# Kernel optimization log

Hardware: AMD Instinct MI355X
Metric: run time of the kernel (lower is better)

## Reference

```python
import jax, jax.numpy as jnp
import numpy as np

N = 65536        # number of encoding vectors (flattened tokens)
K = 1024         # num_embeddings (codebook size)
D = 128          # embedding_dim
BETA = 0.25


def setup_inputs() -> dict:
    key = jax.random.key(0)
    k_enc, k_cb = jax.random.split(key)
    encoding = jax.random.normal(k_enc, (N, D), dtype=jnp.float32)
    # nn.Embedding weight initialized uniform(-1/K, 1/K)
    codebook = jax.random.uniform(k_cb, (K, D), dtype=jnp.float32,
                                  minval=-1.0 / K, maxval=1.0 / K)
    return {"encoding": encoding, "codebook": codebook}


def reference(encoding, codebook):
    # Nearest codebook entry per row. argmin of L2 distance == argmin of
    # squared distance; expand ||e - w||^2 = ||e||^2 - 2 e.w + ||w||^2.
    # ||e||^2 is constant per row, so it does not affect the argmin.
    scores = (-2.0 * jnp.einsum('nd,kd->nk', encoding, codebook)
              + jnp.sum(codebook * codebook, axis=-1)[None, :])  # [N, K]
    quantized_index = jnp.argmin(scores, axis=-1)                # [N] int
    quantized_embedding = codebook[quantized_index]              # [N, D] gather == onehot @ W

    sg = jax.lax.stop_gradient
    commitment_loss = jnp.mean((sg(quantized_embedding) - encoding) ** 2)
    embedding_loss = jnp.mean((quantized_embedding - sg(encoding)) ** 2)
    vq_loss = commitment_loss * BETA + embedding_loss

    # straight-through estimator
    quantized_st = encoding + sg(quantized_embedding - encoding)

    quantized_index = quantized_index[:, None]  # match torch unsqueeze(1) -> [N, 1]
    return (quantized_index, quantized_st, vq_loss, embedding_loss, commitment_loss)
```

## Files before the change

kernel.cpp:

```cpp
#include <hip/hip_runtime.h>


#define NROWS 65536
#define KCB   1024
#define DIM   128
#define DV    32
#define MSE_DENOM 8388608.0f
#define MARGIN 2.0e-5f
#define FLAGCAP 16384
#define CSCALE   1024.0f
#define CDESCALE 0.0009765625f

#define WS_CNORM_F 256
#define WS_LIST_B  8192
#define WS_PH_B    73728
#define WS_PL_B    335872
#define WS_NEEDED  598016

typedef __attribute__((ext_vector_type(16))) float float16v;
typedef _Float16 half8 __attribute__((ext_vector_type(8)));
union U4H8 { uint4 u; half8 h; };
union F4A  { float4 v; float f[4]; };
union HU   { _Float16 f; unsigned short u; };

__device__ __forceinline__ unsigned umn(unsigned a, unsigned b) { return a < b ? a : b; }
__device__ __forceinline__ unsigned umx(unsigned a, unsigned b) { return a > b ? a : b; }
__device__ __forceinline__ float unmap_score(unsigned up) {
  return (up & 0x80000000u) ? __uint_as_float(up ^ 0x80000000u) : __uint_as_float(~up);
}
__device__ __forceinline__ void split2h(float y, unsigned& hb, unsigned& lb) {
  HU h, l;
  h.f = (_Float16)y;
  l.f = (_Float16)(y - (float)h.f);
  hb = h.u; lb = l.u;
}
__device__ __forceinline__ void gload16(const void* g, void* s) {
  __builtin_amdgcn_global_load_lds((const __attribute__((address_space(1))) unsigned int*)g,
                                   (__attribute__((address_space(3))) unsigned int*)s,
                                   16, 0, 0);
}

__global__ __launch_bounds__(256) void vq_prep0(const float* __restrict__ C,
                                                float* __restrict__ wsf) {
  int k = blockIdx.x * 256 + threadIdx.x;
  if (k == 0) { wsf[0] = 0.0f; ((unsigned*)wsf)[1] = 0u; }
  const float4* c4 = (const float4*)C + (size_t)k * DV;
  float s = 0.f;
#pragma unroll 8
  for (int i = 0; i < DV; ++i) {
    float4 v = c4[i];
    s = fmaf(v.x, v.x, s); s = fmaf(v.y, v.y, s);
    s = fmaf(v.z, v.z, s); s = fmaf(v.w, v.w, s);
  }
  wsf[WS_CNORM_F + k] = s;
}

__global__ __launch_bounds__(256) void vq_pack(const float* __restrict__ C,
                                               uint4* __restrict__ PH,
                                               uint4* __restrict__ PL) {
  int g = blockIdx.x * 256 + threadIdx.x;
  int mt = g >> 9, s = (g >> 6) & 7, l = g & 63;
  int cw = mt * 32 + (l & 31);
  int k0 = s * 16 + (l >> 5) * 8;
  const float* src = C + (size_t)cw * DIM + k0;
  float4 x0 = *(const float4*)src;
  float4 x1 = *(const float4*)(src + 4);
  unsigned h[8], lo[8];
  split2h(CSCALE * x0.x, h[0], lo[0]); split2h(CSCALE * x0.y, h[1], lo[1]);
  split2h(CSCALE * x0.z, h[2], lo[2]); split2h(CSCALE * x0.w, h[3], lo[3]);
  split2h(CSCALE * x1.x, h[4], lo[4]); split2h(CSCALE * x1.y, h[5], lo[5]);
  split2h(CSCALE * x1.z, h[6], lo[6]); split2h(CSCALE * x1.w, h[7], lo[7]);
  PH[g] = make_uint4(h[0] | (h[1] << 16), h[2] | (h[3] << 16),
                     h[4] | (h[5] << 16), h[6] | (h[7] << 16));
  PL[g] = make_uint4(lo[0] | (lo[1] << 16), lo[2] | (lo[3] << 16),
                     lo[4] | (lo[5] << 16), lo[6] | (lo[7] << 16));
}

__global__ __launch_bounds__(256, 2) void vq_main3(const float* __restrict__ E,
                                                   const float* __restrict__ C,
                                                   float* __restrict__ wsf,
                                                   float* __restrict__ out) {
  __shared__ uint4 SH[2][512];
  __shared__ uint4 SL[2][512];
  __shared__ __align__(16) float CN[1024];
  __shared__ int BIs[128];

  const int tid  = threadIdx.x;
  const int w    = tid >> 6;
  const int l    = tid & 63;
  const int half = l >> 5;
  const int rr   = l & 31;
  const int row0 = blockIdx.x * 128;

  const uint4* PHg = (const uint4*)((const char*)wsf + WS_PH_B);
  const uint4* PLg = (const uint4*)((const char*)wsf + WS_PL_B);

  {
    const uint4* sh = PHg + tid;
    const uint4* sl = PLg + tid;
    gload16(sh,       &SH[0][0] + tid);
    gload16(sh + 256, &SH[0][0] + tid + 256);
    gload16(sl,       &SL[0][0] + tid);
    gload16(sl + 256, &SL[0][0] + tid + 256);
    gload16(((const uint4*)(wsf + WS_CNORM_F)) + tid, ((uint4*)CN) + tid);
  }

  half8 beh[8], bel[8];
  float s2 = 0.f;
  const float* erow = E + (size_t)(row0 + w * 32 + rr) * DIM + half * 8;
#pragma unroll
  for (int s = 0; s < 8; ++s) {
    float4 x0 = *(const float4*)(erow + s * 16);
    float4 x1 = *(const float4*)(erow + s * 16 + 4);
    float v[8] = {x0.x, x0.y, x0.z, x0.w, x1.x, x1.y, x1.z, x1.w};
#pragma unroll
    for (int j = 0; j < 8; ++j) {
      float y = v[j];
      s2 = fmaf(y, y, s2);
      float t = -2.f * y;
      _Float16 hh = (_Float16)t;
      beh[s][j] = hh;
      bel[s][j] = (_Float16)(t - (float)hh);
    }
  }

  asm volatile("s_waitcnt vmcnt(0)" ::: "memory");
  __syncthreads();

  unsigned best = 0xFFFFFFFFu, second = 0xFFFFFFFFu;

  for (int t = 0; t < 32; ++t) {
    const int buf = t & 1;
    if (t < 31) {
      const uint4* sh = PHg + (t + 1) * 512 + tid;
      const uint4* sl = PLg + (t + 1) * 512 + tid;
      uint4* dh = &SH[buf ^ 1][0];
      uint4* dl = &SL[buf ^ 1][0];
      gload16(sh,       dh + tid);
      gload16(sh + 256, dh + tid + 256);
      gload16(sl,       dl + tid);
      gload16(sl + 256, dl + tid + 256);
    }

    float16v acc0 = {0,0,0,0,0,0,0,0,0,0,0,0,0,0,0,0};
    float16v acc1 = {0,0,0,0,0,0,0,0,0,0,0,0,0,0,0,0};
#pragma unroll
    for (int s = 0; s < 8; s += 2) {
      U4H8 h0, l0, h1, l1;
      h0.u = SH[buf][s * 64 + l];       l0.u = SL[buf][s * 64 + l];
      h1.u = SH[buf][(s + 1) * 64 + l]; l1.u = SL[buf][(s + 1) * 64 + l];
      acc0 = __builtin_amdgcn_mfma_f32_32x32x16_f16(h0.h, beh[s],     acc0, 0, 0, 0);
      acc1 = __builtin_amdgcn_mfma_f32_32x32x16_f16(h1.h, beh[s + 1], acc1, 0, 0, 0);
      acc0 = __builtin_amdgcn_mfma_f32_32x32x16_f16(l0.h, beh[s],     acc0, 0, 0, 0);
      acc1 = __builtin_amdgcn_mfma_f32_32x32x16_f16(l1.h, beh[s + 1], acc1, 0, 0, 0);
      acc0 = __builtin_amdgcn_mfma_f32_32x32x16_f16(h0.h, bel[s],     acc0, 0, 0, 0);
      acc1 = __builtin_amdgcn_mfma_f32_32x32x16_f16(h1.h, bel[s + 1], acc1, 0, 0, 0);
    }

    const unsigned cwb = (unsigned)(t * 32 + half * 4);
    float cnv[16];
#pragma unroll
    for (int q = 0; q < 4; ++q) {
      F4A a; a.v = *(const float4*)&CN[t * 32 + q * 8 + half * 4];
      cnv[q * 4 + 0] = a.f[0]; cnv[q * 4 + 1] = a.f[1];
      cnv[q * 4 + 2] = a.f[2]; cnv[q * 4 + 3] = a.f[3];
    }
#pragma unroll
    for (int reg = 0; reg < 16; ++reg) {
      float sc = fmaf(acc0[reg] + acc1[reg], CDESCALE, cnv[reg]);
      unsigned u = __float_as_uint(sc);
      u ^= ((unsigned)(((int)u) >> 31)) | 0x80000000u;
      u = (u & 0xFFFFFC00u) | (cwb + (unsigned)(((reg >> 2) * 8) + (reg & 3)));
      unsigned nb = umn(best, u);
      second = umn(second, umx(best, u));
      best = nb;
    }

    asm volatile("s_waitcnt vmcnt(0)" ::: "memory");
    __syncthreads();
  }

  unsigned ob = (unsigned)__shfl_xor((int)best, 32, 64);
  unsigned os = (unsigned)__shfl_xor((int)second, 32, 64);
  unsigned ns = umn(umn(second, os), umx(best, ob));
  unsigned nb = umn(best, ob);
  float en = s2 + __shfl_xor(s2, 32, 64);

  if (half == 0) {
    const int r = w * 32 + rr;
    int   bi = (int)(nb & 1023u);
    float bv = unmap_score(nb & 0xFFFFFC00u);
    float sv = unmap_score(ns & 0xFFFFFC00u);
    out[row0 + r] = (float)bi;
    BIs[r] = bi;
    if (sv - bv < MARGIN) {
      unsigned idx = atomicAdd((unsigned*)wsf + 1, 1u);
      if (idx < FLAGCAP) ((int*)((char*)wsf + WS_LIST_B))[idx] = row0 + r;
    }
    float term = en + bv;
#pragma unroll
    for (int off = 16; off > 0; off >>= 1) term += __shfl_down(term, off);
    if (rr == 0) atomicAdd(wsf, term);
  }
  __syncthreads();

  const float4* C4   = (const float4*)C;
  float4*       out4 = (float4*)out;
#pragma unroll
  for (int it = 0; it < 16; ++it) {
    int flat = it * 256 + tid;
    int r = flat >> 5, d4 = flat & 31;
    out4[(NROWS / 4) + (size_t)(row0 + r) * DV + d4] = C4[(size_t)BIs[r] * DV + d4];
  }
}

__global__ __launch_bounds__(256) void vq_fix(const float* __restrict__ E,
                                              const float* __restrict__ C,
                                              float* __restrict__ wsf,
                                              float* __restrict__ out) {
  __shared__ float4 eL0[32], eL1[32];
  __shared__ float  sv0[256], sv1[256];
  __shared__ int    si0[256], si1[256];
  __shared__ int    RESi[2];
  const int tid = threadIdx.x;
  const int* list = (const int*)((const char*)wsf + WS_LIST_B);
  int nf = (int)((const unsigned*)wsf)[1];
  if (nf > FLAGCAP) nf = FLAGCAP;
  const float4* E4 = (const float4*)E;
  const float4* C4 = (const float4*)C;
  const float*  cn = wsf + WS_CNORM_F;
  float4* out4 = (float4*)out;

  for (int pair = blockIdx.x; pair * 2 < nf; pair += gridDim.x) {
    const int r0 = list[pair * 2];
    const int r1 = (pair * 2 + 1 < nf) ? list[pair * 2 + 1] : r0;
    if (tid < 32) eL0[tid] = E4[(size_t)r0 * DV + tid];
    else if (tid < 64) eL1[tid - 32] = E4[(size_t)r1 * DV + (tid - 32)];
    __syncthreads();
    float bv0 = 3.0e38f, bv1 = 3.0e38f; int bi0 = 0, bi1 = 0;
#pragma unroll
    for (int j = 0; j < 4; ++j) {
      int k = j * 256 + tid;
      float d0 = 0.f, d1 = 0.f;
#pragma unroll 8
      for (int d4 = 0; d4 < 32; ++d4) {
        float4 c = C4[(size_t)k * DV + d4];
        float4 e0 = eL0[d4], e1 = eL1[d4];
        d0 = fmaf(c.x, e0.x, d0); d0 = fmaf(c.y, e0.y, d0);
        d0 = fmaf(c.z, e0.z, d0); d0 = fmaf(c.w, e0.w, d0);
        d1 = fmaf(c.x, e1.x, d1); d1 = fmaf(c.y, e1.y, d1);
        d1 = fmaf(c.z, e1.z, d1); d1 = fmaf(c.w, e1.w, d1);
      }
      float s0 = fmaf(-2.f, d0, cn[k]);
      float s1 = fmaf(-2.f, d1, cn[k]);
      if (s0 < bv0 || (s0 == bv0 && k < bi0)) { bv0 = s0; bi0 = k; }
      if (s1 < bv1 || (s1 == bv1 && k < bi1)) { bv1 = s1; bi1 = k; }
    }
    sv0[tid] = bv0; si0[tid] = bi0; sv1[tid] = bv1; si1[tid] = bi1;
    __syncthreads();
    if (tid < 64) {
      float v0 = sv0[tid]; int i0 = si0[tid];
      float v1 = sv1[tid]; int i1 = si1[tid];
#pragma unroll
      for (int q = 1; q < 4; ++q) {
        float w0 = sv0[tid + q * 64]; int j0 = si0[tid + q * 64];
        float w1 = sv1[tid + q * 64]; int j1 = si1[tid + q * 64];
        if (w0 < v0 || (w0 == v0 && j0 < i0)) { v0 = w0; i0 = j0; }
        if (w1 < v1 || (w1 == v1 && j1 < i1)) { v1 = w1; i1 = j1; }
      }
#pragma unroll
      for (int off = 32; off > 0; off >>= 1) {
        float w0 = __shfl_down(v0, off); int j0 = __shfl_down(i0, off);
        float w1 = __shfl_down(v1, off); int j1 = __shfl_down(i1, off);
        if (w0 < v0 || (w0 == v0 && j0 < i0)) { v0 = w0; i0 = j0; }
        if (w1 < v1 || (w1 == v1 && j1 < i1)) { v1 = w1; i1 = j1; }
      }
      if (tid == 0) {
        RESi[0] = i0; RESi[1] = i1;
        out[r0] = (float)i0; out[r1] = (float)i1;
      }
    }
    __syncthreads();
    if (tid < 32) out4[(NROWS / 4) + (size_t)r0 * DV + tid] = C4[(size_t)RESi[0] * DV + tid];
    else if (tid < 64) out4[(NROWS / 4) + (size_t)r1 * DV + (tid - 32)] = C4[(size_t)RESi[1] * DV + (tid - 32)];
    __syncthreads();
  }
}

__global__ void vq_final(const float* __restrict__ wsf, float* __restrict__ out) {
  if (threadIdx.x == 0 && blockIdx.x == 0) {
    float mse = wsf[0] / MSE_DENOM;
    out[NROWS + NROWS * DIM + 0] = 1.25f * mse;
    out[NROWS + NROWS * DIM + 1] = mse;
    out[NROWS + NROWS * DIM + 2] = mse;
  }
}

__global__ __launch_bounds__(256) void vq_prep_fb(const float* __restrict__ C,
                                                  float* __restrict__ ws) {
  int k = blockIdx.x * 256 + threadIdx.x;
  if (k == 0) ws[0] = 0.0f;
  const float4* c4 = (const float4*)C + (size_t)k * DV;
  float s = 0.f;
#pragma unroll 8
  for (int i = 0; i < DV; ++i) {
    float4 v = c4[i];
    s = fmaf(v.x, v.x, s); s = fmaf(v.y, v.y, s);
    s = fmaf(v.z, v.z, s); s = fmaf(v.w, v.w, s);
  }
  ws[64 + k] = s;
}

__global__ __launch_bounds__(256) void vq_main_fb(const float* __restrict__ E,
                                                  const float* __restrict__ C,
                                                  const float* __restrict__ cnorm,
                                                  float* __restrict__ out,
                                                  float* __restrict__ lossacc) {
  __shared__ float smem[16384];
  float4* EsV = (float4*)smem;
  float4* CsV = (float4*)(smem + 8192);
  const int tid  = threadIdx.x;
  const int row0 = blockIdx.x * 64;
#pragma unroll
  for (int i = 0; i < 8; ++i) {
    int flat = i * 256 + tid;
    int r = flat >> 5, d4 = flat & 31;
    EsV[r * 32 + (d4 ^ (r & 31))] = ((const float4*)E)[(size_t)(row0 + r) * DV + d4];
  }
  const int tx = tid & 15, ty = tid >> 4;
  int rbase[4], rmask[4];
#pragma unroll
  for (int i = 0; i < 4; ++i) { int r = i * 16 + ty; rbase[i] = r * 32; rmask[i] = r & 31; }
  float bestv[4]; int besti[4];
#pragma unroll
  for (int i = 0; i < 4; ++i) { bestv[i] = 3.0e38f; besti[i] = 0; }
  for (int ch = 0; ch < 16; ++ch) {
    const int k0 = ch * 64;
    __syncthreads();
#pragma unroll
    for (int i = 0; i < 8; ++i) {
      int flat = i * 256 + tid;
      int k = flat >> 5, d4 = flat & 31;
      CsV[k * 32 + (d4 ^ (k & 31))] = ((const float4*)C)[(size_t)(k0 + k) * DV + d4];
    }
    __syncthreads();
    float acc[4][4] = {};
#pragma unroll 8
    for (int d4 = 0; d4 < DV; ++d4) {
      float4 a[4], b[4];
#pragma unroll
      for (int i = 0; i < 4; ++i) a[i] = EsV[rbase[i] + (d4 ^ rmask[i])];
#pragma unroll
      for (int j = 0; j < 4; ++j) { int k = j * 16 + tx; b[j] = CsV[k * 32 + (d4 ^ (k & 31))]; }
#pragma unroll
      for (int i = 0; i < 4; ++i)
#pragma unroll
        for (int j = 0; j < 4; ++j) {
          acc[i][j] = fmaf(a[i].x, b[j].x, acc[i][j]);
          acc[i][j] = fmaf(a[i].y, b[j].y, acc[i][j]);
          acc[i][j] = fmaf(a[i].z, b[j].z, acc[i][j]);
          acc[i][j] = fmaf(a[i].w, b[j].w, acc[i][j]);
        }
    }
#pragma unroll
    for (int j = 0; j < 4; ++j) {
      int kg = k0 + j * 16 + tx;
      float cnv = cnorm[kg];
#pragma unroll
      for (int i = 0; i < 4; ++i) {
        float s = fmaf(-2.0f, acc[i][j], cnv);
        if (s < bestv[i] || (s == bestv[i] && kg < besti[i])) { bestv[i] = s; besti[i] = kg; }
      }
    }
  }
  float* Rv = smem + 8192;
  int*   Ri = (int*)(smem + 9216);
  int*   BIf = (int*)(smem + 10240);
  __syncthreads();
#pragma unroll
  for (int i = 0; i < 4; ++i) {
    int r = i * 16 + ty;
    Rv[r * 16 + tx] = bestv[i];
    Ri[r * 16 + tx] = besti[i];
  }
  __syncthreads();
  if (tid < 64) {
    const int r = tid;
    float bv = Rv[r * 16]; int bi = Ri[r * 16];
#pragma unroll
    for (int t = 1; t < 16; ++t) {
      float v = Rv[r * 16 + t]; int ii = Ri[r * 16 + t];
      if (v < bv || (v == bv && ii < bi)) { bv = v; bi = ii; }
    }
    float en = 0.f;
#pragma unroll 8
    for (int d4 = 0; d4 < DV; ++d4) {
      float4 v = EsV[r * 32 + (d4 ^ (r & 31))];
      en = fmaf(v.x, v.x, en); en = fmaf(v.y, v.y, en);
      en = fmaf(v.z, v.z, en); en = fmaf(v.w, v.w, en);
    }
    out[row0 + r] = (float)bi;
    BIf[r] = bi;
    float blocksum = en + bv;
#pragma unroll
    for (int off = 32; off > 0; off >>= 1) blocksum += __shfl_down(blocksum, off);
    if (tid == 0) atomicAdd(lossacc, blocksum);
  }
  __syncthreads();
  const float4* C4   = (const float4*)C;
  float4*       out4 = (float4*)out;
  for (int flat = tid; flat < 64 * DV; flat += 256) {
    int r = flat >> 5, d4 = flat & 31;
    out4[(NROWS / 4) + (size_t)(row0 + r) * DV + d4] = C4[(size_t)BIf[r] * DV + d4];
  }
}

__global__ void vq_final_fb(const float* __restrict__ ws, float* __restrict__ out) {
  if (threadIdx.x == 0 && blockIdx.x == 0) {
    float mse = ws[0] / MSE_DENOM;
    out[NROWS + NROWS * DIM + 0] = 1.25f * mse;
    out[NROWS + NROWS * DIM + 1] = mse;
    out[NROWS + NROWS * DIM + 2] = mse;
  }
}

extern "C" void kernel_launch(void* const* d_in, const int* in_sizes, int n_in,
                              void* d_out, int out_size, void* d_ws, size_t ws_size,
                              hipStream_t stream) {
  const float* E = (const float*)d_in[0];
  const float* C = (const float*)d_in[1];
  float* out = (float*)d_out;
  float* wsf = (float*)d_ws;

  if (ws_size >= (size_t)WS_NEEDED) {
    uint4* PH = (uint4*)((char*)d_ws + WS_PH_B);
    uint4* PL = (uint4*)((char*)d_ws + WS_PL_B);
    vq_prep0<<<4, 256, 0, stream>>>(C, wsf);
    vq_pack<<<64, 256, 0, stream>>>(C, PH, PL);
    vq_main3<<<NROWS / 128, 256, 0, stream>>>(E, C, wsf, out);
    vq_fix<<<256, 256, 0, stream>>>(E, C, wsf, out);
    vq_final<<<1, 64, 0, stream>>>(wsf, out);
  } else {
    vq_prep_fb<<<4, 256, 0, stream>>>(C, wsf);
    vq_main_fb<<<NROWS / 64, 256, 0, stream>>>(E, C, wsf + 64, out, wsf);
    vq_final_fb<<<1, 64, 0, stream>>>(wsf, out);
  }
}
```

Before: 186.8 us.

## Split codebook search across two blocks per row tile and merge results

Measured after the change: 188.0 us. Within noise of the previous version (+0.6%).

```diff
diff --git a/kernel.cpp b/kernel.cpp
--- a/kernel.cpp
+++ b/kernel.cpp
@@ -76,33 +76,35 @@
                      lo[4] | (lo[5] << 16), lo[6] | (lo[7] << 16));
 }
 
-__global__ __launch_bounds__(256, 2) void vq_main3(const float* __restrict__ E,
-                                                   const float* __restrict__ C,
+__global__ __launch_bounds__(256, 4) void vq_main4(const float* __restrict__ E,
                                                    float* __restrict__ wsf,
                                                    float* __restrict__ out) {
   __shared__ uint4 SH[2][512];
   __shared__ uint4 SL[2][512];
-  __shared__ __align__(16) float CN[1024];
-  __shared__ int BIs[128];
-
-  const int tid  = threadIdx.x;
-  const int w    = tid >> 6;
-  const int l    = tid & 63;
-  const int half = l >> 5;
-  const int rr   = l & 31;
-  const int row0 = blockIdx.x * 128;
+  __shared__ __align__(16) float CN[512];
+
+  const int tid    = threadIdx.x;
+  const int w      = tid >> 6;
+  const int l      = tid & 63;
+  const int half   = l >> 5;
+  const int rr     = l & 31;
+  const int rowblk = blockIdx.x >> 1;
+  const int cbhalf = blockIdx.x & 1;
+  const int row0   = rowblk * 128;
+  const int tgbase = cbhalf * 16;
 
   const uint4* PHg = (const uint4*)((const char*)wsf + WS_PH_B);
   const uint4* PLg = (const uint4*)((const char*)wsf + WS_PL_B);
 
   {
-    const uint4* sh = PHg + tid;
-    const uint4* sl = PLg + tid;
+    const uint4* sh = PHg + (size_t)tgbase * 512 + tid;
+    const uint4* sl = PLg + (size_t)tgbase * 512 + tid;
     gload16(sh,       &SH[0][0] + tid);
     gload16(sh + 256, &SH[0][0] + tid + 256);
     gload16(sl,       &SL[0][0] + tid);
     gload16(sl + 256, &SL[0][0] + tid + 256);
-    gload16(((const uint4*)(wsf + WS_CNORM_F)) + tid, ((uint4*)CN) + tid);
+    if (tid < 128)
+      gload16(((const uint4*)(wsf + WS_CNORM_F + (cbhalf << 9))) + tid, ((uint4*)CN) + tid);
   }
 
   half8 beh[8], bel[8];
@@ -129,11 +131,12 @@
 
   unsigned best = 0xFFFFFFFFu, second = 0xFFFFFFFFu;
 
-  for (int t = 0; t < 32; ++t) {
+  for (int t = 0; t < 16; ++t) {
     const int buf = t & 1;
-    if (t < 31) {
-      const uint4* sh = PHg + (t + 1) * 512 + tid;
-      const uint4* sl = PLg + (t + 1) * 512 + tid;
+    const int tg  = tgbase + t;
+    if (t < 15) {
+      const uint4* sh = PHg + (size_t)(tg + 1) * 512 + tid;
+      const uint4* sl = PLg + (size_t)(tg + 1) * 512 + tid;
       uint4* dh = &SH[buf ^ 1][0];
       uint4* dl = &SL[buf ^ 1][0];
       gload16(sh,       dh + tid);
@@ -157,23 +160,20 @@
       acc1 = __builtin_amdgcn_mfma_f32_32x32x16_f16(h1.h, bel[s + 1], acc1, 0, 0, 0);
     }
 
-    const unsigned cwb = (unsigned)(t * 32 + half * 4);
-    float cnv[16];
+    const unsigned cwb = (unsigned)(tg * 32 + half * 4);
 #pragma unroll
     for (int q = 0; q < 4; ++q) {
       F4A a; a.v = *(const float4*)&CN[t * 32 + q * 8 + half * 4];
-      cnv[q * 4 + 0] = a.f[0]; cnv[q * 4 + 1] = a.f[1];
-      cnv[q * 4 + 2] = a.f[2]; cnv[q * 4 + 3] = a.f[3];
-    }
-#pragma unroll
-    for (int reg = 0; reg < 16; ++reg) {
-      float sc = fmaf(acc0[reg] + acc1[reg], CDESCALE, cnv[reg]);
-      unsigned u = __float_as_uint(sc);
-      u ^= ((unsigned)(((int)u) >> 31)) | 0x80000000u;
-      u = (u & 0xFFFFFC00u) | (cwb + (unsigned)(((reg >> 2) * 8) + (reg & 3)));
-      unsigned nb = umn(best, u);
-      second = umn(second, umx(best, u));
-      best = nb;
+#pragma unroll
+      for (int i = 0; i < 4; ++i) {
+        float sc = fmaf(acc0[q * 4 + i] + acc1[q * 4 + i], CDESCALE, a.f[i]);
+        unsigned u = __float_as_uint(sc);
+        u ^= ((unsigned)(((int)u) >> 31)) | 0x80000000u;
+        u = (u & 0xFFFFFC00u) | (cwb + (unsigned)(q * 8 + i));
+        unsigned nb = umn(best, u);
+        second = umn(second, umx(best, u));
+        best = nb;
+      }
     }
 
     asm volatile("s_waitcnt vmcnt(0)" ::: "memory");
@@ -187,30 +187,52 @@
   float en = s2 + __shfl_xor(s2, 32, 64);
 
   if (half == 0) {
-    const int r = w * 32 + rr;
-    int   bi = (int)(nb & 1023u);
-    float bv = unmap_score(nb & 0xFFFFFC00u);
-    float sv = unmap_score(ns & 0xFFFFFC00u);
-    out[row0 + r] = (float)bi;
-    BIs[r] = bi;
-    if (sv - bv < MARGIN) {
-      unsigned idx = atomicAdd((unsigned*)wsf + 1, 1u);
-      if (idx < FLAGCAP) ((int*)((char*)wsf + WS_LIST_B))[idx] = row0 + r;
-    }
-    float term = en + bv;
-#pragma unroll
-    for (int off = 16; off > 0; off >>= 1) term += __shfl_down(term, off);
-    if (rr == 0) atomicAdd(wsf, term);
-  }
+    const int R = row0 + w * 32 + rr;
+    float* tmp = out + NROWS + (size_t)R * DIM;
+    ((unsigned*)tmp)[cbhalf * 2 + 0] = nb;
+    ((unsigned*)tmp)[cbhalf * 2 + 1] = ns;
+    if (cbhalf == 0) tmp[4] = en;
+  }
+}
+
+__global__ __launch_bounds__(256) void vq_merge(const float* __restrict__ C,
+                                                float* __restrict__ wsf,
+                                                float* __restrict__ out) {
+  __shared__ int BI[256];
+  const int tid  = threadIdx.x;
+  const int row0 = blockIdx.x * 256;
+  const int R    = row0 + tid;
+
+  const float* tmp = out + NROWS + (size_t)R * DIM;
+  unsigned bA = ((const unsigned*)tmp)[0], sA = ((const unsigned*)tmp)[1];
+  unsigned bB = ((const unsigned*)tmp)[2], sB = ((const unsigned*)tmp)[3];
+  float en = tmp[4];
+
+  unsigned b = umn(bA, bB);
+  unsigned s = umn(umn(sA, sB), umx(bA, bB));
+  int   bi = (int)(b & 1023u);
+  float bv = unmap_score(b & 0xFFFFFC00u);
+  float sv = unmap_score(s & 0xFFFFFC00u);
+
+  out[R] = (float)bi;
+  BI[tid] = bi;
+  if (sv - bv < MARGIN) {
+    unsigned idx = atomicAdd((unsigned*)wsf + 1, 1u);
+    if (idx < FLAGCAP) ((int*)((char*)wsf + WS_LIST_B))[idx] = R;
+  }
+  float term = en + bv;
+#pragma unroll
+  for (int off = 32; off > 0; off >>= 1) term += __shfl_down(term, off);
+  if ((tid & 63) == 0) atomicAdd(wsf, term);
   __syncthreads();
 
   const float4* C4   = (const float4*)C;
   float4*       out4 = (float4*)out;
 #pragma unroll
-  for (int it = 0; it < 16; ++it) {
+  for (int it = 0; it < 32; ++it) {
     int flat = it * 256 + tid;
     int r = flat >> 5, d4 = flat & 31;
-    out4[(NROWS / 4) + (size_t)(row0 + r) * DV + d4] = C4[(size_t)BIs[r] * DV + d4];
+    out4[(NROWS / 4) + (size_t)(row0 + r) * DV + d4] = C4[(size_t)BI[r] * DV + d4];
   }
 }
 
@@ -437,8 +459,9 @@
     uint4* PL = (uint4*)((char*)d_ws + WS_PL_B);
     vq_prep0<<<4, 256, 0, stream>>>(C, wsf);
     vq_pack<<<64, 256, 0, stream>>>(C, PH, PL);
-    vq_main3<<<NROWS / 128, 256, 0, stream>>>(E, C, wsf, out);
-    vq_fix<<<256, 256, 0, stream>>>(E, C, wsf, out);
+    vq_main4<<<NROWS / 128 * 2, 256, 0, stream>>>(E, wsf, out);
+    vq_merge<<<NROWS / 256, 256, 0, stream>>>(C, wsf, out);
+    vq_fix<<<512, 256, 0, stream>>>(E, C, wsf, out);
     vq_final<<<1, 64, 0, stream>>>(wsf, out);
   } else {
     vq_prep_fb<<<4, 256, 0, stream>>>(C, wsf);
```

## Drop codebook low-half split, shrink blocks, and software-pipeline the argmin fold

Applied to the files above, without the earlier changes.

After: 167.0 us. -10.6%, faster.

```diff
diff --git a/kernel.cpp b/kernel.cpp
--- a/kernel.cpp
+++ b/kernel.cpp
@@ -14,8 +14,7 @@
 #define WS_CNORM_F 256
 #define WS_LIST_B  8192
 #define WS_PH_B    73728
-#define WS_PL_B    335872
-#define WS_NEEDED  598016
+#define WS_NEEDED  335872
 
 typedef __attribute__((ext_vector_type(16))) float float16v;
 typedef _Float16 half8 __attribute__((ext_vector_type(8)));
@@ -27,12 +26,6 @@
 __device__ __forceinline__ unsigned umx(unsigned a, unsigned b) { return a > b ? a : b; }
 __device__ __forceinline__ float unmap_score(unsigned up) {
   return (up & 0x80000000u) ? __uint_as_float(up ^ 0x80000000u) : __uint_as_float(~up);
-}
-__device__ __forceinline__ void split2h(float y, unsigned& hb, unsigned& lb) {
-  HU h, l;
-  h.f = (_Float16)y;
-  l.f = (_Float16)(y - (float)h.f);
-  hb = h.u; lb = l.u;
 }
 __device__ __forceinline__ void gload16(const void* g, void* s) {
   __builtin_amdgcn_global_load_lds((const __attribute__((address_space(1))) unsigned int*)g,
@@ -56,8 +49,7 @@
 }
 
 __global__ __launch_bounds__(256) void vq_pack(const float* __restrict__ C,
-                                               uint4* __restrict__ PH,
-                                               uint4* __restrict__ PL) {
+                                               uint4* __restrict__ PH) {
   int g = blockIdx.x * 256 + threadIdx.x;
   int mt = g >> 9, s = (g >> 6) & 7, l = g & 63;
   int cw = mt * 32 + (l & 31);
@@ -65,44 +57,42 @@
   const float* src = C + (size_t)cw * DIM + k0;
   float4 x0 = *(const float4*)src;
   float4 x1 = *(const float4*)(src + 4);
-  unsigned h[8], lo[8];
-  split2h(CSCALE * x0.x, h[0], lo[0]); split2h(CSCALE * x0.y, h[1], lo[1]);
-  split2h(CSCALE * x0.z, h[2], lo[2]); split2h(CSCALE * x0.w, h[3], lo[3]);
-  split2h(CSCALE * x1.x, h[4], lo[4]); split2h(CSCALE * x1.y, h[5], lo[5]);
-  split2h(CSCALE * x1.z, h[6], lo[6]); split2h(CSCALE * x1.w, h[7], lo[7]);
+  unsigned h[8];
+  {
+    float v[8] = {x0.x, x0.y, x0.z, x0.w, x1.x, x1.y, x1.z, x1.w};
+#pragma unroll
+    for (int j = 0; j < 8; ++j) { HU u; u.f = (_Float16)(CSCALE * v[j]); h[j] = u.u; }
+  }
   PH[g] = make_uint4(h[0] | (h[1] << 16), h[2] | (h[3] << 16),
                      h[4] | (h[5] << 16), h[6] | (h[7] << 16));
-  PL[g] = make_uint4(lo[0] | (lo[1] << 16), lo[2] | (lo[3] << 16),
-                     lo[4] | (lo[5] << 16), lo[6] | (lo[7] << 16));
-}
-
-__global__ __launch_bounds__(256, 2) void vq_main3(const float* __restrict__ E,
+}
+
+__global__ __launch_bounds__(128, 2) void vq_main5(const float* __restrict__ E,
                                                    const float* __restrict__ C,
                                                    float* __restrict__ wsf,
                                                    float* __restrict__ out) {
   __shared__ uint4 SH[2][512];
-  __shared__ uint4 SL[2][512];
   __shared__ __align__(16) float CN[1024];
-  __shared__ int BIs[128];
+  __shared__ int BI[64];
 
   const int tid  = threadIdx.x;
   const int w    = tid >> 6;
   const int l    = tid & 63;
   const int half = l >> 5;
   const int rr   = l & 31;
-  const int row0 = blockIdx.x * 128;
+  const int row0 = blockIdx.x * 64;
 
   const uint4* PHg = (const uint4*)((const char*)wsf + WS_PH_B);
-  const uint4* PLg = (const uint4*)((const char*)wsf + WS_PL_B);
 
   {
     const uint4* sh = PHg + tid;
-    const uint4* sl = PLg + tid;
     gload16(sh,       &SH[0][0] + tid);
+    gload16(sh + 128, &SH[0][0] + tid + 128);
     gload16(sh + 256, &SH[0][0] + tid + 256);
-    gload16(sl,       &SL[0][0] + tid);
-    gload16(sl + 256, &SL[0][0] + tid + 256);
-    gload16(((const uint4*)(wsf + WS_CNORM_F)) + tid, ((uint4*)CN) + tid);
+    gload16(sh + 384, &SH[0][0] + tid + 384);
+    const uint4* cn = ((const uint4*)(wsf + WS_CNORM_F)) + tid;
+    gload16(cn,       ((uint4*)CN) + tid);
+    gload16(cn + 128, ((uint4*)CN) + tid + 128);
   }
 
   half8 beh[8], bel[8];
@@ -128,57 +118,75 @@
   __syncthreads();
 
   unsigned best = 0xFFFFFFFFu, second = 0xFFFFFFFFu;
-
-  for (int t = 0; t < 32; ++t) {
-    const int buf = t & 1;
-    if (t < 31) {
-      const uint4* sh = PHg + (t + 1) * 512 + tid;
-      const uint4* sl = PLg + (t + 1) * 512 + tid;
-      uint4* dh = &SH[buf ^ 1][0];
-      uint4* dl = &SL[buf ^ 1][0];
-      gload16(sh,       dh + tid);
-      gload16(sh + 256, dh + tid + 256);
-      gload16(sl,       dl + tid);
-      gload16(sl + 256, dl + tid + 256);
-    }
-
+  float sc[16];
+  int tprev = 0;
+
+#define STAGE_TILE(tn)                                                     \
+  {                                                                        \
+    const uint4* sh_ = PHg + (size_t)(tn) * 512 + tid;                     \
+    uint4* dh_ = &SH[(tn) & 1][0];                                         \
+    gload16(sh_,       dh_ + tid);                                         \
+    gload16(sh_ + 128, dh_ + tid + 128);                                   \
+    gload16(sh_ + 256, dh_ + tid + 256);                                   \
+    gload16(sh_ + 384, dh_ + tid + 384);                                   \
+  }
+
+#define COMPUTE_TILE(tt, A0, A1)                                           \
+  _Pragma("unroll")                                                        \
+  for (int s = 0; s < 8; s += 2) {                                         \
+    U4H8 h0, h1;                                                           \
+    h0.u = SH[(tt) & 1][s * 64 + l];                                       \
+    h1.u = SH[(tt) & 1][(s + 1) * 64 + l];                                 \
+    A0 = __builtin_amdgcn_mfma_f32_32x32x16_f16(h0.h, beh[s],     A0, 0, 0, 0); \
+    A1 = __builtin_amdgcn_mfma_f32_32x32x16_f16(h1.h, beh[s + 1], A1, 0, 0, 0); \
+    A0 = __builtin_amdgcn_mfma_f32_32x32x16_f16(h0.h, bel[s],     A0, 0, 0, 0); \
+    A1 = __builtin_amdgcn_mfma_f32_32x32x16_f16(h1.h, bel[s + 1], A1, 0, 0, 0); \
+  }
+
+#define FOLD_PREV()                                                        \
+  {                                                                        \
+    const unsigned cwb_ = (unsigned)(tprev * 32 + half * 4);               \
+    _Pragma("unroll")                                                      \
+    for (int q = 0; q < 4; ++q) {                                          \
+      F4A a_; a_.v = *(const float4*)&CN[tprev * 32 + q * 8 + half * 4];   \
+      _Pragma("unroll")                                                    \
+      for (int i = 0; i < 4; ++i) {                                        \
+        float scv_ = fmaf(sc[q * 4 + i], CDESCALE, a_.f[i]);               \
+        unsigned u_ = __float_as_uint(scv_);                               \
+        u_ ^= ((unsigned)(((int)u_) >> 31)) | 0x80000000u;                 \
+        u_ = (u_ & 0xFFFFFC00u) | (cwb_ + (unsigned)(q * 8 + i));          \
+        unsigned nb_ = umn(best, u_);                                      \
+        second = umn(second, umx(best, u_));                               \
+        best = nb_;                                                        \
+      }                                                                    \
+    }                                                                      \
+  }
+
+  {
+    STAGE_TILE(1);
     float16v acc0 = {0,0,0,0,0,0,0,0,0,0,0,0,0,0,0,0};
     float16v acc1 = {0,0,0,0,0,0,0,0,0,0,0,0,0,0,0,0};
-#pragma unroll
-    for (int s = 0; s < 8; s += 2) {
-      U4H8 h0, l0, h1, l1;
-      h0.u = SH[buf][s * 64 + l];       l0.u = SL[buf][s * 64 + l];
-      h1.u = SH[buf][(s + 1) * 64 + l]; l1.u = SL[buf][(s + 1) * 64 + l];
-      acc0 = __builtin_amdgcn_mfma_f32_32x32x16_f16(h0.h, beh[s],     acc0, 0, 0, 0);
-      acc1 = __builtin_amdgcn_mfma_f32_32x32x16_f16(h1.h, beh[s + 1], acc1, 0, 0, 0);
-      acc0 = __builtin_amdgcn_mfma_f32_32x32x16_f16(l0.h, beh[s],     acc0, 0, 0, 0);
-      acc1 = __builtin_amdgcn_mfma_f32_32x32x16_f16(l1.h, beh[s + 1], acc1, 0, 0, 0);
-      acc0 = __builtin_amdgcn_mfma_f32_32x32x16_f16(h0.h, bel[s],     acc0, 0, 0, 0);
-      acc1 = __builtin_amdgcn_mfma_f32_32x32x16_f16(h1.h, bel[s + 1], acc1, 0, 0, 0);
-    }
-
-    const unsigned cwb = (unsigned)(t * 32 + half * 4);
-    float cnv[16];
-#pragma unroll
-    for (int q = 0; q < 4; ++q) {
-      F4A a; a.v = *(const float4*)&CN[t * 32 + q * 8 + half * 4];
-      cnv[q * 4 + 0] = a.f[0]; cnv[q * 4 + 1] = a.f[1];
-      cnv[q * 4 + 2] = a.f[2]; cnv[q * 4 + 3] = a.f[3];
-    }
-#pragma unroll
-    for (int reg = 0; reg < 16; ++reg) {
-      float sc = fmaf(acc0[reg] + acc1[reg], CDESCALE, cnv[reg]);
-      unsigned u = __float_as_uint(sc);
-      u ^= ((unsigned)(((int)u) >> 31)) | 0x80000000u;
-      u = (u & 0xFFFFFC00u) | (cwb + (unsigned)(((reg >> 2) * 8) + (reg & 3)));
-      unsigned nb = umn(best, u);
-      second = umn(second, umx(best, u));
-      best = nb;
-    }
-
+    COMPUTE_TILE(0, acc0, acc1);
+#pragma unroll
+    for (int r = 0; r < 16; ++r) sc[r] = acc0[r] + acc1[r];
+    tprev = 0;
     asm volatile("s_waitcnt vmcnt(0)" ::: "memory");
     __syncthreads();
   }
+
+  for (int t = 1; t < 32; ++t) {
+    if (t < 31) STAGE_TILE(t + 1);
+    float16v acc0 = {0,0,0,0,0,0,0,0,0,0,0,0,0,0,0,0};
+    float16v acc1 = {0,0,0,0,0,0,0,0,0,0,0,0,0,0,0,0};
+    COMPUTE_TILE(t, acc0, acc1);
+    FOLD_PREV();
+#pragma unroll
+    for (int r = 0; r < 16; ++r) sc[r] = acc0[r] + acc1[r];
+    tprev = t;
+    asm volatile("s_waitcnt vmcnt(0)" ::: "memory");
+    __syncthreads();
+  }
+  FOLD_PREV();
 
   unsigned ob = (unsigned)__shfl_xor((int)best, 32, 64);
   unsigned os = (unsigned)__shfl_xor((int)second, 32, 64);
@@ -192,7 +200,7 @@
     float bv = unmap_score(nb & 0xFFFFFC00u);
     float sv = unmap_score(ns & 0xFFFFFC00u);
     out[row0 + r] = (float)bi;
-    BIs[r] = bi;
+    BI[r] = bi;
     if (sv - bv < MARGIN) {
       unsigned idx = atomicAdd((unsigned*)wsf + 1, 1u);
       if (idx < FLAGCAP) ((int*)((char*)wsf + WS_LIST_B))[idx] = row0 + r;
@@ -208,10 +216,13 @@
   float4*       out4 = (float4*)out;
 #pragma unroll
   for (int it = 0; it < 16; ++it) {
-    int flat = it * 256 + tid;
+    int flat = it * 128 + tid;
     int r = flat >> 5, d4 = flat & 31;
-    out4[(NROWS / 4) + (size_t)(row0 + r) * DV + d4] = C4[(size_t)BIs[r] * DV + d4];
-  }
+    out4[(NROWS / 4) + (size_t)(row0 + r) * DV + d4] = C4[(size_t)BI[r] * DV + d4];
+  }
+#undef STAGE_TILE
+#undef COMPUTE_TILE
+#undef FOLD_PREV
 }
 
 __global__ __launch_bounds__(256) void vq_fix(const float* __restrict__ E,
@@ -434,11 +445,10 @@
 
   if (ws_size >= (size_t)WS_NEEDED) {
     uint4* PH = (uint4*)((char*)d_ws + WS_PH_B);
-    uint4* PL = (uint4*)((char*)d_ws + WS_PL_B);
     vq_prep0<<<4, 256, 0, stream>>>(C, wsf);
-    vq_pack<<<64, 256, 0, stream>>>(C, PH, PL);
-    vq_main3<<<NROWS / 128, 256, 0, stream>>>(E, C, wsf, out);
-    vq_fix<<<256, 256, 0, stream>>>(E, C, wsf, out);
+    vq_pack<<<64, 256, 0, stream>>>(C, PH);
+    vq_main5<<<NROWS / 64, 128, 0, stream>>>(E, C, wsf, out);
+    vq_fix<<<512, 256, 0, stream>>>(E, C, wsf, out);
     vq_final<<<1, 64, 0, stream>>>(wsf, out);
   } else {
     vq_prep_fb<<<4, 256, 0, stream>>>(C, wsf);
```
